# Kernel optimization log

Measured on AMD Instinct MI355X. Metric: run time of the kernel, lower is better.

Reference implementation:

```python
import jax, jax.numpy as jnp
import numpy as np

B, L, E, H = 2, 2048, 1024, 16
D = E // H  # head dim = 64


def setup_inputs() -> dict:
    key = jax.random.key(0)
    ks = jax.random.split(key, 10)
    s = 0.02
    return {
        "xt": jax.random.normal(ks[0], (B, L, E), jnp.float32),
        "xs": jax.random.normal(ks[1], (B, L, E), jnp.float32),
        "Wt": jax.random.normal(ks[2], (E, 3 * E), jnp.float32) * s,  # t_attn weight (x @ Wt)
        "bt": jnp.zeros((3 * E,), jnp.float32),
        "Ws": jax.random.normal(ks[3], (E, 2 * E), jnp.float32) * s,  # s_attn weight
        "bs": jnp.zeros((2 * E,), jnp.float32),
        "Wc": jax.random.normal(ks[4], (E, E), jnp.float32) * s,      # c_proj weight
        "bc": jnp.zeros((E,), jnp.float32),
        "lam_ts": jnp.ones((1,), jnp.float32),
        "lam_st": jnp.ones((1,), jnp.float32),
        "lam_ss": jnp.ones((1,), jnp.float32),
    }


def _heads(x):
    # (B, L, E) -> (B, H, L, D)
    return x.reshape(B, L, H, D).transpose(0, 2, 1, 3)


def reference(xt, xs, Wt, bt, Ws, bs, Wc, bc, lam_ts, lam_st, lam_ss):
    qt, kt, vt = jnp.split(xt @ Wt + bt, 3, axis=2)
    qs, ks = jnp.split(xs @ Ws + bs, 2, axis=2)
    qt, kt, vt, qs, ks = map(_heads, (qt, kt, vt, qs, ks))

    # 4-way disentangled scores; fuse the 4 matmuls into 2 by combining keys:
    # qt@kt^T + lam_ts*qt@ks^T = qt @ (kt + lam_ts*ks)^T
    # lam_st*qs@kt^T + lam_ss*qs@ks^T = qs @ (lam_st*kt + lam_ss*ks)^T
    k1 = kt + lam_ts[0] * ks
    k2 = lam_st[0] * kt + lam_ss[0] * ks
    att = (jnp.einsum('bhqd,bhkd->bhqk', qt, k1)
           + jnp.einsum('bhqd,bhkd->bhqk', qs, k2)) * (1.0 / np.sqrt(D))
    att = jax.nn.softmax(att, axis=-1)
    y = jnp.einsum('bhqk,bhkd->bhqd', att, vt)  # (B, H, L, D)
    y = y.transpose(0, 2, 1, 3).reshape(B, L, E)
    return y @ Wc + bc
```

## Files before the change

kernel.cpp:

```cpp
#include <hip/hip_runtime.h>
#include <math.h>

#define LQ 2048
#define EQ 1024
#define M_ROWS 4096
#define BH 32

typedef _Float16 f16x8 __attribute__((ext_vector_type(8)));
typedef _Float16 f16x4 __attribute__((ext_vector_type(4)));
typedef float f32x4 __attribute__((ext_vector_type(4)));
typedef float f32x16 __attribute__((ext_vector_type(16)));

#define QSCALE 0.1803368801111204f

__device__ __forceinline__ void async_ld16(const _Float16* g, _Float16* l) {
  __builtin_amdgcn_global_load_lds(
      (const __attribute__((address_space(1))) unsigned int*)g,
      (__attribute__((address_space(3))) unsigned int*)l, 16, 0, 0);
}

__global__ __launch_bounds__(256) void convert_x(
    const float* __restrict__ xt, const float* __restrict__ xs,
    _Float16* __restrict__ xt16, _Float16* __restrict__ xs16) {
  int i = blockIdx.x * 256 + threadIdx.x;
  const float* s; _Float16* d; size_t off;
  if (i < 524288) { s = xt; d = xt16; off = (size_t)i * 8; }
  else            { s = xs; d = xs16; off = (size_t)(i - 524288) * 8; }
  float4 a = *(const float4*)&s[off];
  float4 b = *(const float4*)&s[off + 4];
  f16x8 h;
  h[0] = (_Float16)a.x; h[1] = (_Float16)a.y; h[2] = (_Float16)a.z; h[3] = (_Float16)a.w;
  h[4] = (_Float16)b.x; h[5] = (_Float16)b.y; h[6] = (_Float16)b.z; h[7] = (_Float16)b.w;
  *(f16x8*)&d[off] = h;
}

__global__ __launch_bounds__(256) void transpose_w(
    const float* __restrict__ Wt, const float* __restrict__ Ws,
    const float* __restrict__ Wc,
    _Float16* __restrict__ WtT, _Float16* __restrict__ WsT,
    _Float16* __restrict__ WcT) {
  __shared__ float T[32][33];
  int tx = threadIdx.x & 31, ty = threadIdx.x >> 5;
  int c0 = blockIdx.x * 32;
  int k0 = blockIdx.y * 32;
  const float* W; _Float16* D; int Nw, cl;
  if (c0 < 3072)      { W = Wt; D = WtT; Nw = 3072; cl = c0; }
  else if (c0 < 5120) { W = Ws; D = WsT; Nw = 2048; cl = c0 - 3072; }
  else                { W = Wc; D = WcT; Nw = 1024; cl = c0 - 5120; }
#pragma unroll
  for (int j = 0; j < 4; ++j)
    T[ty + j * 8][tx] = W[(size_t)(k0 + ty + j * 8) * Nw + cl + tx];
  __syncthreads();
#pragma unroll
  for (int j = 0; j < 4; ++j)
    D[(size_t)(cl + ty + j * 8) * 1024 + k0 + tx] = (_Float16)T[tx][ty + j * 8];
}

__global__ __launch_bounds__(256) void gemm_bt(
    const _Float16* __restrict__ A, const _Float16* __restrict__ Bm,
    const float* __restrict__ bias,
    float* __restrict__ outf, _Float16* __restrict__ q16,
    _Float16* __restrict__ k16, _Float16* __restrict__ v16,
    const float* __restrict__ lam_ts, const float* __restrict__ lam_st,
    const float* __restrict__ lam_ss,
    int mode) {
  __shared__ _Float16 Al[128 * 32];
  __shared__ _Float16 Bl[128 * 32];

  const int tid = threadIdx.x;
  const int w = tid >> 6;
  const int lane = tid & 63;
  const int quad = lane >> 4;
  const int l15 = lane & 15;
  const int wm = w >> 1, wn = w & 1;

  const _Float16* Ab = A;
  const _Float16* Bb = Bm;
  int m0 = blockIdx.y * 128;
  const int n0 = blockIdx.x * 128;
  int bsel = 0;
  bool vpath = false;
  if (mode == 0 && blockIdx.y >= 32) {
    int by2 = blockIdx.y - 32;
    bsel = by2 >> 3;
    m0 = (by2 & 7) * 128;
    Ab = Bm + (size_t)2048 * 1024;
    Bb = A + (size_t)bsel * 2048 * 1024;
    vpath = true;
  }

  const int srow = lane >> 2;
  const int schunk = ((lane & 3) ^ ((lane >> 3) & 3)) * 8;

  float lts = 0.f, lst = 0.f, lss = 0.f;
  if (mode == 1) { lts = lam_ts[0]; lst = lam_st[0]; lss = lam_ss[0]; }

  f32x4 acc[4][4];
#pragma unroll
  for (int mb = 0; mb < 4; ++mb)
#pragma unroll
    for (int nb = 0; nb < 4; ++nb) acc[mb][nb] = (f32x4){0.f, 0.f, 0.f, 0.f};

  const int key = (l15 >> 1) & 3;

  for (int kt = 0; kt < 1024; kt += 32) {
    __syncthreads();
#pragma unroll
    for (int i = 0; i < 2; ++i) {
      int rt = w * 32 + i * 16;
      async_ld16(&Ab[(size_t)(m0 + rt + srow) * 1024 + kt + schunk], &Al[rt * 32]);
      async_ld16(&Bb[(size_t)(n0 + rt + srow) * 1024 + kt + schunk], &Bl[rt * 32]);
    }
    __syncthreads();

    f16x8 af[4], bf[4];
    const int pc = (quad ^ key) * 8;
#pragma unroll
    for (int mb = 0; mb < 4; ++mb)
      af[mb] = *(f16x8*)&Al[(wm * 64 + mb * 16 + l15) * 32 + pc];
#pragma unroll
    for (int nb = 0; nb < 4; ++nb)
      bf[nb] = *(f16x8*)&Bl[(wn * 64 + nb * 16 + l15) * 32 + pc];
#pragma unroll
    for (int mb = 0; mb < 4; ++mb)
#pragma unroll
      for (int nb = 0; nb < 4; ++nb)
        acc[mb][nb] = __builtin_amdgcn_mfma_f32_16x16x32_f16(af[mb], bf[nb], acc[mb][nb], 0, 0, 0);
  }

#pragma unroll
  for (int mb = 0; mb < 4; ++mb)
#pragma unroll
    for (int nb = 0; nb < 4; ++nb)
#pragma unroll
      for (int r = 0; r < 4; ++r) {
        int row = m0 + wm * 64 + mb * 16 + quad * 4 + r;
        int col = n0 + wn * 64 + nb * 16 + l15;
        if (vpath) {
          float val = acc[mb][nb][r] + bias[2048 + row];
          v16[(size_t)(bsel * 1024 + row) * 2048 + col] = (_Float16)val;
        } else {
          float val = acc[mb][nb][r] + bias[col];
          if (mode == 2) {
            outf[(size_t)row * 1024 + col] = val;
          } else {
            int bb = row >> 11, ll = row & 2047;
            int which = col >> 10, e = col & 1023;
            int hh = e >> 6, dd = e & 63;
            size_t rowhd = (size_t)(bb * 16 + hh) * 2048 + ll;
            if (mode == 0) {
              if (which == 0) q16[rowhd * 128 + dd] = (_Float16)(val * QSCALE);
              else            k16[rowhd * 128 + dd] = (_Float16)val;
            } else {
              if (which == 0) {
                q16[rowhd * 128 + 64 + dd] = (_Float16)(val * QSCALE);
              } else {
                float ktv = (float)k16[rowhd * 128 + dd];
                float ksv = val;
                k16[rowhd * 128 + dd]      = (_Float16)(ktv + lts * ksv);
                k16[rowhd * 128 + 64 + dd] = (_Float16)(lst * ktv + lss * ksv);
              }
            }
          }
        }
      }
}

__global__ __launch_bounds__(256, 2) void flash_attn_mfma(
    const _Float16* __restrict__ qcat, const _Float16* __restrict__ kcat,
    const _Float16* __restrict__ vT, _Float16* __restrict__ y) {
  const int bh = blockIdx.y;
  const int qt0 = blockIdx.x * 128;
  const int b = bh >> 4, h = bh & 15;
  const _Float16* Qg = qcat + (size_t)bh * LQ * 128;
  const _Float16* Kg = kcat + (size_t)bh * LQ * 128;
  const _Float16* Vg = vT + (size_t)bh * 64 * LQ;

  __shared__ _Float16 Ksh0[64 * 128];
  __shared__ _Float16 Ksh1[64 * 128];
  __shared__ _Float16 Vsh0[64 * 64];
  __shared__ _Float16 Vsh1[64 * 64];
  __shared__ _Float16 Psh[4 * 32 * 72];

  const int tid = threadIdx.x;
  const int w = tid >> 6;
  const int lane = tid & 63;
  const int half = lane >> 5;
  const int l31 = lane & 31;

  f16x8 qf[8];
#pragma unroll
  for (int db = 0; db < 8; ++db)
    qf[db] = *(const f16x8*)&Qg[(size_t)(qt0 + w * 32 + l31) * 128 + db * 16 + half * 8];

  float m_i = -INFINITY;
  float l_i = 0.f;
  f32x16 O[2];
#pragma unroll
  for (int nt = 0; nt < 2; ++nt)
#pragma unroll
    for (int r = 0; r < 16; ++r) O[nt][r] = 0.f;

  _Float16* Pw = &Psh[w * 32 * 72];

  auto dma = [&](int t, _Float16* Kd, _Float16* Vd) {
#pragma unroll
    for (int a = 0; a < 4; ++a) {
      int row = w * 16 + a * 4 + (lane >> 4);
      int sc = (lane & 15) ^ (row & 7);
      async_ld16(&Kg[(size_t)(t + row) * 128 + sc * 8], &Kd[(w * 16 + a * 4) * 128]);
    }
#pragma unroll
    for (int a = 0; a < 2; ++a) {
      int row = w * 16 + a * 8 + (lane >> 3);
      int sc = (lane & 7) ^ (row & 7);
      async_ld16(&Vg[(size_t)row * LQ + t + sc * 8], &Vd[(w * 16 + a * 8) * 64]);
    }
  };

  auto compute = [&](const _Float16* Ks, const _Float16* Vs) {
    f32x16 S[2];
#pragma unroll
    for (int kb = 0; kb < 2; ++kb)
#pragma unroll
      for (int r = 0; r < 16; ++r) S[kb][r] = 0.f;
#pragma unroll
    for (int db = 0; db < 8; ++db) {
      const int pc = ((db * 2 + half) ^ (lane & 7)) * 8;
      f16x8 af[2];
#pragma unroll
      for (int kb = 0; kb < 2; ++kb)
        af[kb] = *(const f16x8*)&Ks[(kb * 32 + l31) * 128 + pc];
#pragma unroll
      for (int kb = 0; kb < 2; ++kb)
        S[kb] = __builtin_amdgcn_mfma_f32_32x32x16_f16(af[kb], qf[db], S[kb], 0, 0, 0);
    }

    float mx = -INFINITY;
#pragma unroll
    for (int kb = 0; kb < 2; ++kb)
#pragma unroll
      for (int r = 0; r < 16; ++r) mx = fmaxf(mx, S[kb][r]);
    mx = fmaxf(mx, __shfl_xor(mx, 32));
    float m_new = fmaxf(m_i, mx);
    float alpha = __builtin_amdgcn_exp2f(m_i - m_new);
    float s = 0.f;
#pragma unroll
    for (int kb = 0; kb < 2; ++kb)
#pragma unroll
      for (int r = 0; r < 16; ++r) {
        float p = __builtin_amdgcn_exp2f(S[kb][r] - m_new);
        S[kb][r] = p;
        s += p;
      }
    s += __shfl_xor(s, 32);
    l_i = l_i * alpha + s;
    m_i = m_new;

#pragma unroll
    for (int kb = 0; kb < 2; ++kb)
#pragma unroll
      for (int rg = 0; rg < 4; ++rg) {
        f16x4 p4;
#pragma unroll
        for (int i = 0; i < 4; ++i) p4[i] = (_Float16)S[kb][rg * 4 + i];
        *(f16x4*)&Pw[l31 * 72 + kb * 32 + rg * 8 + half * 4] = p4;
      }

#pragma unroll
    for (int nt = 0; nt < 2; ++nt)
#pragma unroll
      for (int r = 0; r < 16; ++r) O[nt][r] *= alpha;

#pragma unroll
    for (int kb = 0; kb < 4; ++kb) {
      f16x8 pb = *(const f16x8*)&Pw[l31 * 72 + kb * 16 + half * 8];
      f16x8 av[2];
#pragma unroll
      for (int nt = 0; nt < 2; ++nt) {
        int dim = nt * 32 + l31;
        int pc = ((kb * 2 + half) ^ (dim & 7)) * 8;
        av[nt] = *(const f16x8*)&Vs[dim * 64 + pc];
      }
#pragma unroll
      for (int nt = 0; nt < 2; ++nt)
        O[nt] = __builtin_amdgcn_mfma_f32_32x32x16_f16(av[nt], pb, O[nt], 0, 0, 0);
    }
  };

  dma(0, Ksh0, Vsh0);
  for (int t = 0; t < LQ; t += 128) {
    __syncthreads();
    dma(t + 64, Ksh1, Vsh1);
    compute(Ksh0, Vsh0);
    __syncthreads();
    if (t + 128 < LQ) dma(t + 128, Ksh0, Vsh0);
    compute(Ksh1, Vsh1);
  }

  float inv = 1.f / l_i;
  int qrow = qt0 + w * 32 + l31;
#pragma unroll
  for (int nt = 0; nt < 2; ++nt)
#pragma unroll
    for (int rg = 0; rg < 4; ++rg) {
      f16x4 o4;
#pragma unroll
      for (int i = 0; i < 4; ++i) o4[i] = (_Float16)(O[nt][rg * 4 + i] * inv);
      int dim = nt * 32 + rg * 8 + half * 4;
      *(f16x4*)&y[((size_t)b * LQ + qrow) * EQ + h * 64 + dim] = o4;
    }
}

extern "C" void kernel_launch(void* const* d_in, const int* in_sizes, int n_in,
                              void* d_out, int out_size, void* d_ws, size_t ws_size,
                              hipStream_t stream) {
  const float* xt = (const float*)d_in[0];
  const float* xs = (const float*)d_in[1];
  const float* Wt = (const float*)d_in[2];
  const float* bt = (const float*)d_in[3];
  const float* Ws = (const float*)d_in[4];
  const float* bs = (const float*)d_in[5];
  const float* Wc = (const float*)d_in[6];
  const float* bc = (const float*)d_in[7];
  const float* lam_ts = (const float*)d_in[8];
  const float* lam_st = (const float*)d_in[9];
  const float* lam_ss = (const float*)d_in[10];
  float* out = (float*)d_out;

  _Float16* w16 = (_Float16*)d_ws;
  _Float16* xt16 = w16;
  _Float16* xs16 = xt16 + 4194304;
  _Float16* WtT  = xs16 + 4194304;
  _Float16* WsT  = WtT + 3145728;
  _Float16* WcT  = WsT + 2097152;
  _Float16* qcat = WcT + 1048576;
  _Float16* kcat = qcat + 8388608;
  _Float16* vbufT = kcat + 8388608;
  _Float16* ybuf = vbufT + 4194304;

  convert_x<<<4096, 256, 0, stream>>>(xt, xs, xt16, xs16);
  transpose_w<<<dim3(192, 32), 256, 0, stream>>>(Wt, Ws, Wc, WtT, WsT, WcT);
  gemm_bt<<<dim3(16, 48), 256, 0, stream>>>(
      xt16, WtT, bt, nullptr, qcat, kcat, vbufT, nullptr, nullptr, nullptr, 0);
  gemm_bt<<<dim3(16, 32), 256, 0, stream>>>(
      xs16, WsT, bs, nullptr, qcat, kcat, nullptr, lam_ts, lam_st, lam_ss, 1);
  flash_attn_mfma<<<dim3(16, 32), 256, 0, stream>>>(qcat, kcat, vbufT, ybuf);
  gemm_bt<<<dim3(8, 32), 256, 0, stream>>>(
      ybuf, WcT, bc, out, nullptr, nullptr, nullptr, nullptr, nullptr, nullptr, 2);
}
```

Before: 308.0 us.

## Merge projection GEMMs, fold lambda mixing into Q, shuffle P through registers

The two prep kernels become one launch. The two QKV projection GEMMs become a single launch that writes raw kt/ks and qt/qs halves. This removes the read-modify-write of K in the second GEMM and the serial dependency between those launches. The lambda mixing is re-expressed algebraically on the query side inside the attention kernel, so each Q row is combined once in registers. The attention P tile is now redistributed with cross-lane shuffles instead of a round trip through shared memory, which frees LDS. This costs extra shuffle instructions and adds a Q-side conversion that rounds through fp16.

```diff
diff --git a/kernel.cpp b/kernel.cpp
--- a/kernel.cpp
+++ b/kernel.cpp
@@ -8,6 +8,7 @@
 
 typedef _Float16 f16x8 __attribute__((ext_vector_type(8)));
 typedef _Float16 f16x4 __attribute__((ext_vector_type(4)));
+typedef _Float16 f16x2 __attribute__((ext_vector_type(2)));
 typedef float f32x4 __attribute__((ext_vector_type(4)));
 typedef float f32x16 __attribute__((ext_vector_type(16)));
 
@@ -19,51 +20,51 @@
       (__attribute__((address_space(3))) unsigned int*)l, 16, 0, 0);
 }
 
-__global__ __launch_bounds__(256) void convert_x(
+__global__ __launch_bounds__(256) void prep(
     const float* __restrict__ xt, const float* __restrict__ xs,
-    _Float16* __restrict__ xt16, _Float16* __restrict__ xs16) {
-  int i = blockIdx.x * 256 + threadIdx.x;
-  const float* s; _Float16* d; size_t off;
-  if (i < 524288) { s = xt; d = xt16; off = (size_t)i * 8; }
-  else            { s = xs; d = xs16; off = (size_t)(i - 524288) * 8; }
-  float4 a = *(const float4*)&s[off];
-  float4 b = *(const float4*)&s[off + 4];
-  f16x8 h;
-  h[0] = (_Float16)a.x; h[1] = (_Float16)a.y; h[2] = (_Float16)a.z; h[3] = (_Float16)a.w;
-  h[4] = (_Float16)b.x; h[5] = (_Float16)b.y; h[6] = (_Float16)b.z; h[7] = (_Float16)b.w;
-  *(f16x8*)&d[off] = h;
-}
-
-__global__ __launch_bounds__(256) void transpose_w(
     const float* __restrict__ Wt, const float* __restrict__ Ws,
     const float* __restrict__ Wc,
+    _Float16* __restrict__ xt16, _Float16* __restrict__ xs16,
     _Float16* __restrict__ WtT, _Float16* __restrict__ WsT,
     _Float16* __restrict__ WcT) {
-  __shared__ float T[32][33];
-  int tx = threadIdx.x & 31, ty = threadIdx.x >> 5;
-  int c0 = blockIdx.x * 32;
-  int k0 = blockIdx.y * 32;
-  const float* W; _Float16* D; int Nw, cl;
-  if (c0 < 3072)      { W = Wt; D = WtT; Nw = 3072; cl = c0; }
-  else if (c0 < 5120) { W = Ws; D = WsT; Nw = 2048; cl = c0 - 3072; }
-  else                { W = Wc; D = WcT; Nw = 1024; cl = c0 - 5120; }
-#pragma unroll
-  for (int j = 0; j < 4; ++j)
-    T[ty + j * 8][tx] = W[(size_t)(k0 + ty + j * 8) * Nw + cl + tx];
-  __syncthreads();
-#pragma unroll
-  for (int j = 0; j < 4; ++j)
-    D[(size_t)(cl + ty + j * 8) * 1024 + k0 + tx] = (_Float16)T[tx][ty + j * 8];
-}
-
-__global__ __launch_bounds__(256) void gemm_bt(
-    const _Float16* __restrict__ A, const _Float16* __restrict__ Bm,
-    const float* __restrict__ bias,
-    float* __restrict__ outf, _Float16* __restrict__ q16,
-    _Float16* __restrict__ k16, _Float16* __restrict__ v16,
-    const float* __restrict__ lam_ts, const float* __restrict__ lam_st,
-    const float* __restrict__ lam_ss,
-    int mode) {
+  int gb = blockIdx.x;
+  if (gb < 4096) {
+    int i = gb * 256 + threadIdx.x;
+    const float* s; _Float16* d; size_t off;
+    if (i < 524288) { s = xt; d = xt16; off = (size_t)i * 8; }
+    else            { s = xs; d = xs16; off = (size_t)(i - 524288) * 8; }
+    float4 a = *(const float4*)&s[off];
+    float4 b = *(const float4*)&s[off + 4];
+    f16x8 h;
+    h[0] = (_Float16)a.x; h[1] = (_Float16)a.y; h[2] = (_Float16)a.z; h[3] = (_Float16)a.w;
+    h[4] = (_Float16)b.x; h[5] = (_Float16)b.y; h[6] = (_Float16)b.z; h[7] = (_Float16)b.w;
+    *(f16x8*)&d[off] = h;
+  } else {
+    __shared__ float T[32][33];
+    int tb = gb - 4096;
+    int tx = threadIdx.x & 31, ty = threadIdx.x >> 5;
+    int c0 = (tb % 192) * 32;
+    int k0 = (tb / 192) * 32;
+    const float* W; _Float16* D; int Nw, cl;
+    if (c0 < 3072)      { W = Wt; D = WtT; Nw = 3072; cl = c0; }
+    else if (c0 < 5120) { W = Ws; D = WsT; Nw = 2048; cl = c0 - 3072; }
+    else                { W = Wc; D = WcT; Nw = 1024; cl = c0 - 5120; }
+#pragma unroll
+    for (int j = 0; j < 4; ++j)
+      T[ty + j * 8][tx] = W[(size_t)(k0 + ty + j * 8) * Nw + cl + tx];
+    __syncthreads();
+#pragma unroll
+    for (int j = 0; j < 4; ++j)
+      D[(size_t)(cl + ty + j * 8) * 1024 + k0 + tx] = (_Float16)T[tx][ty + j * 8];
+  }
+}
+
+__global__ __launch_bounds__(256) void proj_gemm(
+    const _Float16* __restrict__ xt16, const _Float16* __restrict__ xs16,
+    const _Float16* __restrict__ WtT, const _Float16* __restrict__ WsT,
+    const float* __restrict__ bt, const float* __restrict__ bs,
+    _Float16* __restrict__ q16, _Float16* __restrict__ k16,
+    _Float16* __restrict__ v16) {
   __shared__ _Float16 Al[128 * 32];
   __shared__ _Float16 Bl[128 * 32];
 
@@ -73,27 +74,29 @@
   const int quad = lane >> 4;
   const int l15 = lane & 15;
   const int wm = w >> 1, wn = w & 1;
-
-  const _Float16* Ab = A;
-  const _Float16* Bb = Bm;
-  int m0 = blockIdx.y * 128;
+  const int by = blockIdx.y;
   const int n0 = blockIdx.x * 128;
-  int bsel = 0;
-  bool vpath = false;
-  if (mode == 0 && blockIdx.y >= 32) {
-    int by2 = blockIdx.y - 32;
+
+  const _Float16* Ab;
+  const _Float16* Bb;
+  const float* bias;
+  int m0, bsel = 0, branch;
+  if (by < 32) {
+    branch = 0; Ab = xt16; Bb = WtT; bias = bt; m0 = by * 128;
+  } else if (by < 48) {
+    branch = 1;
+    int by2 = by - 32;
     bsel = by2 >> 3;
     m0 = (by2 & 7) * 128;
-    Ab = Bm + (size_t)2048 * 1024;
-    Bb = A + (size_t)bsel * 2048 * 1024;
-    vpath = true;
+    Ab = WtT + (size_t)2048 * 1024;
+    Bb = xt16 + (size_t)bsel * 2048 * 1024;
+    bias = bt;
+  } else {
+    branch = 2; Ab = xs16; Bb = WsT; bias = bs; m0 = (by - 48) * 128;
   }
 
   const int srow = lane >> 2;
   const int schunk = ((lane & 3) ^ ((lane >> 3) & 3)) * 8;
-
-  float lts = 0.f, lst = 0.f, lss = 0.f;
-  if (mode == 1) { lts = lam_ts[0]; lst = lam_st[0]; lss = lam_ss[0]; }
 
   f32x4 acc[4][4];
 #pragma unroll
@@ -136,39 +139,90 @@
       for (int r = 0; r < 4; ++r) {
         int row = m0 + wm * 64 + mb * 16 + quad * 4 + r;
         int col = n0 + wn * 64 + nb * 16 + l15;
-        if (vpath) {
+        if (branch == 1) {
           float val = acc[mb][nb][r] + bias[2048 + row];
           v16[(size_t)(bsel * 1024 + row) * 2048 + col] = (_Float16)val;
         } else {
           float val = acc[mb][nb][r] + bias[col];
-          if (mode == 2) {
-            outf[(size_t)row * 1024 + col] = val;
-          } else {
-            int bb = row >> 11, ll = row & 2047;
-            int which = col >> 10, e = col & 1023;
-            int hh = e >> 6, dd = e & 63;
-            size_t rowhd = (size_t)(bb * 16 + hh) * 2048 + ll;
-            if (mode == 0) {
-              if (which == 0) q16[rowhd * 128 + dd] = (_Float16)(val * QSCALE);
-              else            k16[rowhd * 128 + dd] = (_Float16)val;
-            } else {
-              if (which == 0) {
-                q16[rowhd * 128 + 64 + dd] = (_Float16)(val * QSCALE);
-              } else {
-                float ktv = (float)k16[rowhd * 128 + dd];
-                float ksv = val;
-                k16[rowhd * 128 + dd]      = (_Float16)(ktv + lts * ksv);
-                k16[rowhd * 128 + 64 + dd] = (_Float16)(lst * ktv + lss * ksv);
-              }
-            }
-          }
+          int bb = row >> 11, ll = row & 2047;
+          int which = col >> 10, e = col & 1023;
+          int hh = e >> 6, dd = e & 63;
+          size_t rowhd = (size_t)(bb * 16 + hh) * 2048 + ll;
+          int off = (branch == 0) ? 0 : 64;
+          if (which == 0) q16[rowhd * 128 + off + dd] = (_Float16)val;
+          else            k16[rowhd * 128 + off + dd] = (_Float16)val;
         }
       }
 }
 
+__global__ __launch_bounds__(256) void cproj_gemm(
+    const _Float16* __restrict__ A, const _Float16* __restrict__ Bm,
+    const float* __restrict__ bias, float* __restrict__ outf) {
+  __shared__ _Float16 Al[128 * 32];
+  __shared__ _Float16 Bl[128 * 32];
+
+  const int tid = threadIdx.x;
+  const int w = tid >> 6;
+  const int lane = tid & 63;
+  const int quad = lane >> 4;
+  const int l15 = lane & 15;
+  const int wm = w >> 1, wn = w & 1;
+  const int m0 = blockIdx.y * 128;
+  const int n0 = blockIdx.x * 128;
+
+  const int srow = lane >> 2;
+  const int schunk = ((lane & 3) ^ ((lane >> 3) & 3)) * 8;
+
+  f32x4 acc[4][4];
+#pragma unroll
+  for (int mb = 0; mb < 4; ++mb)
+#pragma unroll
+    for (int nb = 0; nb < 4; ++nb) acc[mb][nb] = (f32x4){0.f, 0.f, 0.f, 0.f};
+
+  const int key = (l15 >> 1) & 3;
+
+  for (int kt = 0; kt < 1024; kt += 32) {
+    __syncthreads();
+#pragma unroll
+    for (int i = 0; i < 2; ++i) {
+      int rt = w * 32 + i * 16;
+      async_ld16(&A[(size_t)(m0 + rt + srow) * 1024 + kt + schunk], &Al[rt * 32]);
+      async_ld16(&Bm[(size_t)(n0 + rt + srow) * 1024 + kt + schunk], &Bl[rt * 32]);
+    }
+    __syncthreads();
+
+    f16x8 af[4], bf[4];
+    const int pc = (quad ^ key) * 8;
+#pragma unroll
+    for (int mb = 0; mb < 4; ++mb)
+      af[mb] = *(f16x8*)&Al[(wm * 64 + mb * 16 + l15) * 32 + pc];
+#pragma unroll
+    for (int nb = 0; nb < 4; ++nb)
+      bf[nb] = *(f16x8*)&Bl[(wn * 64 + nb * 16 + l15) * 32 + pc];
+#pragma unroll
+    for (int mb = 0; mb < 4; ++mb)
+#pragma unroll
+      for (int nb = 0; nb < 4; ++nb)
+        acc[mb][nb] = __builtin_amdgcn_mfma_f32_16x16x32_f16(af[mb], bf[nb], acc[mb][nb], 0, 0, 0);
+  }
+
+#pragma unroll
+  for (int mb = 0; mb < 4; ++mb)
+#pragma unroll
+    for (int nb = 0; nb < 4; ++nb)
+#pragma unroll
+      for (int r = 0; r < 4; ++r) {
+        int row = m0 + wm * 64 + mb * 16 + quad * 4 + r;
+        int col = n0 + wn * 64 + nb * 16 + l15;
+        outf[(size_t)row * 1024 + col] = acc[mb][nb][r] + bias[col];
+      }
+}
+
 __global__ __launch_bounds__(256, 2) void flash_attn_mfma(
     const _Float16* __restrict__ qcat, const _Float16* __restrict__ kcat,
-    const _Float16* __restrict__ vT, _Float16* __restrict__ y) {
+    const _Float16* __restrict__ vT, _Float16* __restrict__ y,
+    const float* __restrict__ lam_ts, const float* __restrict__ lam_st,
+    const float* __restrict__ lam_ss) {
   const int bh = blockIdx.y;
   const int qt0 = blockIdx.x * 128;
   const int b = bh >> 4, h = bh & 15;
@@ -180,7 +234,6 @@
   __shared__ _Float16 Ksh1[64 * 128];
   __shared__ _Float16 Vsh0[64 * 64];
   __shared__ _Float16 Vsh1[64 * 64];
-  __shared__ _Float16 Psh[4 * 32 * 72];
 
   const int tid = threadIdx.x;
   const int w = tid >> 6;
@@ -188,10 +241,21 @@
   const int half = lane >> 5;
   const int l31 = lane & 31;
 
+  const float lts = lam_ts[0], lst = lam_st[0], lss = lam_ss[0];
+
   f16x8 qf[8];
 #pragma unroll
-  for (int db = 0; db < 8; ++db)
-    qf[db] = *(const f16x8*)&Qg[(size_t)(qt0 + w * 32 + l31) * 128 + db * 16 + half * 8];
+  for (int db = 0; db < 4; ++db) {
+    const _Float16* qp = &Qg[(size_t)(qt0 + w * 32 + l31) * 128 + db * 16 + half * 8];
+    f16x8 a = *(const f16x8*)qp;
+    f16x8 bq = *(const f16x8*)(qp + 64);
+#pragma unroll
+    for (int e = 0; e < 8; ++e) {
+      float fa = (float)a[e], fb = (float)bq[e];
+      qf[db][e]     = (_Float16)(QSCALE * (fa + lst * fb));
+      qf[db + 4][e] = (_Float16)(QSCALE * (lts * fa + lss * fb));
+    }
+  }
 
   float m_i = -INFINITY;
   float l_i = 0.f;
@@ -200,8 +264,6 @@
   for (int nt = 0; nt < 2; ++nt)
 #pragma unroll
     for (int r = 0; r < 16; ++r) O[nt][r] = 0.f;
-
-  _Float16* Pw = &Psh[w * 32 * 72];
 
   auto dma = [&](int t, _Float16* Kd, _Float16* Vd) {
 #pragma unroll
@@ -258,34 +320,48 @@
     m_i = m_new;
 
 #pragma unroll
+    for (int nt = 0; nt < 2; ++nt)
+#pragma unroll
+      for (int r = 0; r < 16; ++r) O[nt][r] *= alpha;
+
+    unsigned pu[2][8];
+#pragma unroll
     for (int kb = 0; kb < 2; ++kb)
 #pragma unroll
-      for (int rg = 0; rg < 4; ++rg) {
-        f16x4 p4;
-#pragma unroll
-        for (int i = 0; i < 4; ++i) p4[i] = (_Float16)S[kb][rg * 4 + i];
-        *(f16x4*)&Pw[l31 * 72 + kb * 32 + rg * 8 + half * 4] = p4;
+      for (int i = 0; i < 8; ++i) {
+        f16x2 t2;
+        t2[0] = (_Float16)S[kb][2 * i];
+        t2[1] = (_Float16)S[kb][2 * i + 1];
+        pu[kb][i] = __builtin_bit_cast(unsigned, t2);
       }
 
 #pragma unroll
-    for (int nt = 0; nt < 2; ++nt)
-#pragma unroll
-      for (int r = 0; r < 16; ++r) O[nt][r] *= alpha;
-
-#pragma unroll
-    for (int kb = 0; kb < 4; ++kb) {
-      f16x8 pb = *(const f16x8*)&Pw[l31 * 72 + kb * 16 + half * 8];
-      f16x8 av[2];
-#pragma unroll
-      for (int nt = 0; nt < 2; ++nt) {
-        int dim = nt * 32 + l31;
-        int pc = ((kb * 2 + half) ^ (dim & 7)) * 8;
-        av[nt] = *(const f16x8*)&Vs[dim * 64 + pc];
+    for (int kb = 0; kb < 2; ++kb)
+#pragma unroll
+      for (int c = 0; c < 2; ++c) {
+        unsigned ulo0 = pu[kb][4 * c + 0], ulo1 = pu[kb][4 * c + 1];
+        unsigned uhi0 = pu[kb][4 * c + 2], uhi1 = pu[kb][4 * c + 3];
+        unsigned rlo0 = (unsigned)__shfl_xor((int)ulo0, 32);
+        unsigned rlo1 = (unsigned)__shfl_xor((int)ulo1, 32);
+        unsigned rhi0 = (unsigned)__shfl_xor((int)uhi0, 32);
+        unsigned rhi1 = (unsigned)__shfl_xor((int)uhi1, 32);
+        union { unsigned u[4]; f16x8 v; } pb;
+        pb.u[0] = half ? rhi0 : ulo0;
+        pb.u[1] = half ? rhi1 : ulo1;
+        pb.u[2] = half ? uhi0 : rlo0;
+        pb.u[3] = half ? uhi1 : rlo1;
+        int kb2 = kb * 2 + c;
+        f16x8 av[2];
+#pragma unroll
+        for (int nt = 0; nt < 2; ++nt) {
+          int dim = nt * 32 + l31;
+          int pc = ((kb2 * 2 + half) ^ (dim & 7)) * 8;
+          av[nt] = *(const f16x8*)&Vs[dim * 64 + pc];
+        }
+#pragma unroll
+        for (int nt = 0; nt < 2; ++nt)
+          O[nt] = __builtin_amdgcn_mfma_f32_32x32x16_f16(av[nt], pb.v, O[nt], 0, 0, 0);
       }
-#pragma unroll
-      for (int nt = 0; nt < 2; ++nt)
-        O[nt] = __builtin_amdgcn_mfma_f32_32x32x16_f16(av[nt], pb, O[nt], 0, 0, 0);
-    }
   };
 
   dma(0, Ksh0, Vsh0);
@@ -339,13 +415,10 @@
   _Float16* vbufT = kcat + 8388608;
   _Float16* ybuf = vbufT + 4194304;
 
-  convert_x<<<4096, 256, 0, stream>>>(xt, xs, xt16, xs16);
-  transpose_w<<<dim3(192, 32), 256, 0, stream>>>(Wt, Ws, Wc, WtT, WsT, WcT);
-  gemm_bt<<<dim3(16, 48), 256, 0, stream>>>(
-      xt16, WtT, bt, nullptr, qcat, kcat, vbufT, nullptr, nullptr, nullptr, 0);
-  gemm_bt<<<dim3(16, 32), 256, 0, stream>>>(
-      xs16, WsT, bs, nullptr, qcat, kcat, nullptr, lam_ts, lam_st, lam_ss, 1);
-  flash_attn_mfma<<<dim3(16, 32), 256, 0, stream>>>(qcat, kcat, vbufT, ybuf);
-  gemm_bt<<<dim3(8, 32), 256, 0, stream>>>(
-      ybuf, WcT, bc, out, nullptr, nullptr, nullptr, nullptr, nullptr, nullptr, 2);
-}
+  prep<<<10240, 256, 0, stream>>>(xt, xs, Wt, Ws, Wc, xt16, xs16, WtT, WsT, WcT);
+  proj_gemm<<<dim3(16, 80), 256, 0, stream>>>(
+      xt16, xs16, WtT, WsT, bt, bs, qcat, kcat, vbufT);
+  flash_attn_mfma<<<dim3(16, 32), 256, 0, stream>>>(
+      qcat, kcat, vbufT, ybuf, lam_ts, lam_st, lam_ss);
+  cproj_gemm<<<dim3(8, 32), 256, 0, stream>>>(ybuf, WcT, bc, out);
+}
```

New measurement: 281.9 us. 8.5% less time.
